# Performance work log

Hardware: AMD Instinct MI355X
Metric: run time of the kernel (lower is better)

Reference implementation:

```python
import jax, jax.numpy as jnp
import numpy as np

NUM_HEADS = 16

def setup_inputs() -> dict:
    key = jax.random.key(0)
    ks = jax.random.split(key, 7)
    B, Nq, Nkv, D = 4, 1024, 4096, 1024
    q = jax.random.normal(ks[0], (B, Nq, D), dtype=jnp.float32)
    kv = jax.random.normal(ks[1], (B, Nkv, D), dtype=jnp.float32)
    # True = padded key; keep position 0 unmasked so no row is fully masked
    mask = jax.random.randint(ks[2], (B, Nkv), 0, 2) > 0
    mask = mask.at[:, 0].set(False)
    s = D ** -0.5
    Wq = jax.random.normal(ks[3], (D, D), dtype=jnp.float32) * s
    Wkv = jax.random.normal(ks[4], (D, 2 * D), dtype=jnp.float32) * s
    Wproj = jax.random.normal(ks[5], (D, D), dtype=jnp.float32) * s
    bproj = jnp.zeros((D,), dtype=jnp.float32)
    return {"q": q, "kv": kv, "key_padding_mask": mask,
            "Wq": Wq, "Wkv": Wkv, "Wproj": Wproj, "bproj": bproj}

def reference(q, kv, key_padding_mask, Wq, Wkv, Wproj, bproj):
    B, Nq, D = q.shape
    Nkv = kv.shape[1]
    H = NUM_HEADS
    hd = D // H
    scale = hd ** -0.5
    # projections (qkv_bias=False)
    qp = (q @ Wq).reshape(B, Nq, H, hd).transpose(0, 2, 1, 3) * scale  # (B,H,Nq,hd)
    kvp = kv @ Wkv  # (B,Nkv,2D); first D -> k, last D -> v
    k = kvp[..., :D].reshape(B, Nkv, H, hd).transpose(0, 2, 1, 3)  # (B,H,Nkv,hd)
    v = kvp[..., D:].reshape(B, Nkv, H, hd).transpose(0, 2, 1, 3)
    attn = jnp.einsum('bhqd,bhkd->bhqk', qp, k)  # (B,H,Nq,Nkv)
    neg_inf = jnp.finfo(attn.dtype).min
    attn = jnp.where(key_padding_mask[:, None, None, :], neg_inf, attn)
    attn = jax.nn.softmax(attn, axis=-1)
    x = jnp.einsum('bhqk,bhkd->bhqd', attn, v)  # (B,H,Nq,hd)
    x = x.transpose(0, 2, 1, 3).reshape(B, Nq, D)
    return x @ Wproj + bproj
```

## Files before the change

kernel.cpp:

```cpp
#include <hip/hip_runtime.h>
#include <hip/hip_bf16.h>
#include <math.h>

#define BB 4
#define NQ 1024
#define NKV 4096
#define DMODEL 1024
#define NH 16
#define HD 64

typedef __attribute__((ext_vector_type(8))) short short8;
typedef __attribute__((ext_vector_type(4))) float floatx4;

__device__ __forceinline__ unsigned short f2bf(float f) {
    __hip_bfloat16 b = __float2bfloat16(f);
    return *reinterpret_cast<unsigned short*>(&b);
}

__device__ __forceinline__ unsigned int pack2bf_rhu(float a, float b) {
    unsigned ua = __builtin_bit_cast(unsigned, a) + 0x8000u;
    unsigned ub = __builtin_bit_cast(unsigned, b) + 0x8000u;
    return (ua >> 16) | (ub & 0xffff0000u);
}

__device__ __forceinline__ void gl_lds16(void* lds, const void* g) {
    __builtin_amdgcn_global_load_lds(
        (const __attribute__((address_space(1))) unsigned int*)g,
        (__attribute__((address_space(3))) unsigned int*)lds, 16, 0, 0);
}

__global__ __launch_bounds__(1024) void maskprep3(const int* __restrict__ mask,
                                                  unsigned short* __restrict__ maskb) {
    __shared__ int s;
    if (threadIdx.x == 0) s = 0;
    __syncthreads();
    int local = 0;
    for (int i = threadIdx.x; i < 4096; i += 1024)
        if (((const unsigned*)mask)[i] > 1u) local = 1;
    if (local) atomicOr(&s, 1);
    __syncthreads();
    const bool bytes = (s != 0);
    for (int i = threadIdx.x; i < BB * NKV; i += 1024) {
        bool m = bytes ? (((const unsigned char*)mask)[i] != 0) : (mask[i] != 0);
        maskb[i] = m ? (unsigned short)0 : (unsigned short)0xFFFFu;
    }
}

__global__ __launch_bounds__(256) void cast_bf16(const float* __restrict__ src,
                                                 unsigned short* __restrict__ dst,
                                                 int n) {
    int i = (blockIdx.x * 256 + threadIdx.x) * 8;
    if (i >= n) return;
    float4 a = *(const float4*)&src[i];
    float4 b = *(const float4*)&src[i + 4];
    short8 v;
    v[0] = (short)f2bf(a.x); v[1] = (short)f2bf(a.y);
    v[2] = (short)f2bf(a.z); v[3] = (short)f2bf(a.w);
    v[4] = (short)f2bf(b.x); v[5] = (short)f2bf(b.y);
    v[6] = (short)f2bf(b.z); v[7] = (short)f2bf(b.w);
    *(short8*)&dst[i] = v;
}

__global__ __launch_bounds__(256) void transpose_cast3(
    const float* __restrict__ Wq, const float* __restrict__ Wkv,
    const float* __restrict__ Wproj,
    unsigned short* __restrict__ WqT, unsigned short* __restrict__ WkvT,
    unsigned short* __restrict__ WprojT)
{
    const float* src; unsigned short* dst; int N;
    if (blockIdx.z == 0)      { src = Wq;    dst = WqT;    N = DMODEL; }
    else if (blockIdx.z == 1) { src = Wkv;   dst = WkvT;   N = 2 * DMODEL; }
    else                      { src = Wproj; dst = WprojT; N = DMODEL; }
    if ((int)blockIdx.x * 64 >= N) return;
    const int K = DMODEL;
    __shared__ unsigned short t[64][72];
    int r0 = blockIdx.y * 64, c0 = blockIdx.x * 64;
    int tid = threadIdx.x;
#pragma unroll
    for (int i = 0; i < 4; i++) {
        int r = i * 16 + (tid >> 4), c = (tid & 15) * 4;
        float4 v = *(const float4*)&src[(size_t)(r0 + r) * N + c0 + c];
        t[c + 0][r] = f2bf(v.x); t[c + 1][r] = f2bf(v.y);
        t[c + 2][r] = f2bf(v.z); t[c + 3][r] = f2bf(v.w);
    }
    __syncthreads();
#pragma unroll
    for (int i = 0; i < 2; i++) {
        int rr = i * 32 + (tid >> 3), cc = (tid & 7) * 8;
        *(uint4*)&dst[(size_t)(c0 + rr) * K + r0 + cc] = *(uint4*)&t[rr][cc];
    }
}

template <int EPI>
__global__ __launch_bounds__(256) void gemm_mfma(
    const unsigned short* __restrict__ A,
    const unsigned short* __restrict__ Bt,
    const float* __restrict__ bias,
    unsigned short* __restrict__ o16,
    unsigned short* __restrict__ oT,
    float* __restrict__ o32,
    int M, int N, int K, float alpha, int m_out_base)
{
    extern __shared__ char smem[];
    unsigned short* As = (unsigned short*)smem;
    unsigned short* Bs = (unsigned short*)(smem + 8192);
    const int tid = threadIdx.x;
    const int wave = tid >> 6, lane = tid & 63;
    const int quad = lane >> 4, l16 = lane & 15;
    const int wm = wave >> 1, wn = wave & 1;
    const int m0 = blockIdx.y * 128, n0 = blockIdx.x * 128;

    const int c0 = wave * 64 + lane, c1 = c0 + 256;
    const int r0s = c0 >> 2, cc0 = (c0 & 3) ^ ((r0s >> 2) & 3);
    const int r1s = c1 >> 2, cc1 = (c1 & 3) ^ ((r1s >> 2) & 3);
    const unsigned short* ag0 = A + (size_t)(m0 + r0s) * K + cc0 * 8;
    const unsigned short* ag1 = A + (size_t)(m0 + r1s) * K + cc1 * 8;
    const unsigned short* bg0 = Bt + (size_t)(n0 + r0s) * K + cc0 * 8;
    const unsigned short* bg1 = Bt + (size_t)(n0 + r1s) * K + cc1 * 8;
    char* AldsW0 = (char*)As + (wave * 64) * 16;
    char* AldsW1 = (char*)As + (256 + wave * 64) * 16;
    char* BldsW0 = (char*)Bs + (wave * 64) * 16;
    char* BldsW1 = (char*)Bs + (256 + wave * 64) * 16;

    int achk[4], bchk[4];
#pragma unroll
    for (int i = 0; i < 4; i++) {
        int ra = wm * 64 + i * 16 + l16;
        achk[i] = ra * 4 + (quad ^ ((ra >> 2) & 3));
        int rb = wn * 64 + i * 16 + l16;
        bchk[i] = rb * 4 + (quad ^ ((rb >> 2) & 3));
    }

    floatx4 acc[4][4];
#pragma unroll
    for (int i = 0; i < 4; i++)
#pragma unroll
        for (int j = 0; j < 4; j++) acc[i][j] = (floatx4)0.0f;

    for (int kt = 0; kt < K; kt += 32) {
        __syncthreads();
        gl_lds16(AldsW0, ag0 + kt);
        gl_lds16(AldsW1, ag1 + kt);
        gl_lds16(BldsW0, bg0 + kt);
        gl_lds16(BldsW1, bg1 + kt);
        __syncthreads();
        short8 af[4], bfr[4];
#pragma unroll
        for (int i = 0; i < 4; i++) af[i] = *(const short8*)&As[achk[i] * 8];
#pragma unroll
        for (int j = 0; j < 4; j++) bfr[j] = *(const short8*)&Bs[bchk[j] * 8];
#pragma unroll
        for (int i = 0; i < 4; i++)
#pragma unroll
            for (int j = 0; j < 4; j++)
                acc[i][j] = __builtin_amdgcn_mfma_f32_16x16x32_bf16(
                    af[i], bfr[j], acc[i][j], 0, 0, 0);
    }

    const int rowbase = m0 + wm * 64;
    const int colbase = n0 + wn * 64;
    if (EPI == 0) {
#pragma unroll
        for (int i = 0; i < 4; i++)
#pragma unroll
            for (int r = 0; r < 4; r++) {
                size_t row = (size_t)(rowbase + i * 16 + quad * 4 + r);
#pragma unroll
                for (int j = 0; j < 4; j++)
                    o16[row * N + colbase + j * 16 + l16] =
                        f2bf(acc[i][j][r] * alpha);
            }
    } else if (EPI == 2) {
        float bv[4];
#pragma unroll
        for (int j = 0; j < 4; j++) bv[j] = bias[colbase + j * 16 + l16];
#pragma unroll
        for (int i = 0; i < 4; i++)
#pragma unroll
            for (int r = 0; r < 4; r++) {
                size_t row = (size_t)(rowbase + i * 16 + quad * 4 + r);
#pragma unroll
                for (int j = 0; j < 4; j++)
                    o32[row * N + colbase + j * 16 + l16] = acc[i][j][r] + bv[j];
            }
    } else {
        if (n0 < DMODEL) {
#pragma unroll
            for (int i = 0; i < 4; i++)
#pragma unroll
                for (int r = 0; r < 4; r++) {
                    int gm = m_out_base + rowbase + i * 16 + quad * 4 + r;
                    int b = gm >> 12, key = gm & (NKV - 1);
                    size_t row = (size_t)(b * NKV + key);
#pragma unroll
                    for (int j = 0; j < 4; j++)
                        o16[row * DMODEL + colbase + j * 16 + l16] =
                            f2bf(acc[i][j][r]);
                }
        } else {
            __syncthreads();
            unsigned short (*scr)[72] =
                (unsigned short(*)[72])(smem + wave * 64 * 72 * 2);
#pragma unroll
            for (int i = 0; i < 4; i++)
#pragma unroll
                for (int j = 0; j < 4; j++)
#pragma unroll
                    for (int r = 0; r < 4; r++)
                        scr[j * 16 + l16][i * 16 + quad * 4 + r] =
                            f2bf(acc[i][j][r]);
            __syncthreads();
            int gmb = m_out_base + rowbase;
            int b = gmb >> 12, key0 = gmb & (NKV - 1);
            int d0 = colbase - DMODEL;
#pragma unroll
            for (int p = 0; p < 8; p++) {
                int rr = p * 8 + (lane >> 3), ch = lane & 7;
                *(uint4*)&oT[((size_t)(b * DMODEL + d0 + rr)) * NKV + key0 + ch * 8] =
                    *(uint4*)&scr[rr][ch * 8];
            }
        }
    }
}

__global__ __launch_bounds__(512, 2) void attn_mfma11(
    const unsigned short* __restrict__ Qb,
    const unsigned short* __restrict__ Kb,
    const unsigned short* __restrict__ VTb,
    const unsigned short* __restrict__ maskb,
    unsigned short* __restrict__ x)
{
    const int lid = blockIdx.y * gridDim.x + blockIdx.x;
    const int xcd = lid & 7, slot = lid >> 3;
    const int bh = xcd * 8 + (slot & 7);
    const int b = bh >> 4, h = bh & 15;
    const int m0 = (slot >> 3) * 128;
    const int tid = threadIdx.x;
    const int wave = tid >> 6, lane = tid & 63;
    const int quad = lane >> 4, l16 = lane & 15;
    const int sp = wave & 3;
    const int g  = wave >> 2;

    __shared__ __align__(16) char smem[55296];
    unsigned short (*k_s)[64][72]  = (unsigned short (*)[64][72])(smem);
    unsigned short (*vT_s)[64][72] = (unsigned short (*)[64][72])(smem + 18432);
    unsigned short (*qp_s)[16][72] = (unsigned short (*)[16][72])(smem + 36864);
    float* comb = (float*)smem;

    const unsigned short* Kbase = Kb + ((size_t)b * NKV) * DMODEL + h * HD;
    const unsigned short* Vbase = VTb + ((size_t)(b * DMODEL + h * HD)) * NKV;

    const int sg  = tid >> 8;
    const int t8  = tid & 255;
    const int sr  = t8 >> 2;
    const int sc  = (t8 & 3) * 16;
    const int key00 = sg * 2048;

    {
        const unsigned short* ks = Kbase + (size_t)(key00 + sr) * DMODEL + sc;
        uint4 a0 = *(const uint4*)ks, a1 = *(const uint4*)(ks + 8);
        const unsigned short* vs = Vbase + (size_t)sr * NKV + key00 + sc;
        uint4 b0 = *(const uint4*)vs, b1 = *(const uint4*)(vs + 8);
        *(uint4*)&k_s[sg][sr][sc]      = a0;
        *(uint4*)&k_s[sg][sr][sc + 8]  = a1;
        *(uint4*)&vT_s[sg][sr][sc]     = b0;
        *(uint4*)&vT_s[sg][sr][sc + 8] = b1;
    }

    short8 bq[2][2];
#pragma unroll
    for (int s = 0; s < 2; s++) {
        const unsigned short* qsrc =
            Qb + ((size_t)(b * NQ + m0 + sp * 32 + s * 16 + l16)) * DMODEL +
            h * HD + quad * 8;
        bq[s][0] = *(const short8*)qsrc;
        bq[s][1] = *(const short8*)(qsrc + 32);
    }

    const unsigned short* mrow = maskb + b * NKV + g * 2048;
    unsigned short* prow = &qp_s[wave][l16][0];

    short8 ones;
#pragma unroll
    for (int e = 0; e < 8; e++) ones[e] = (short)0x3F80;

    floatx4 o[2][4], ol[2];
#pragma unroll
    for (int s = 0; s < 2; s++) {
#pragma unroll
        for (int f = 0; f < 4; f++) o[s][f] = (floatx4)0.0f;
        ol[s] = (floatx4)0.0f;
    }

    __syncthreads();

    for (int i = 0; i < 32; i++) {
        if (i) __syncthreads();
        const bool pf = (i < 31);
        const int nn = key00 + (i + 1) * 64;

        uint4 pk0, pk1;
        if (pf) {
            const unsigned short* ks = Kbase + (size_t)(nn + sr) * DMODEL + sc;
            pk0 = *(const uint4*)ks; pk1 = *(const uint4*)(ks + 8);
        }

        floatx4 st[2][4];
        __builtin_amdgcn_s_setprio(1);
#pragma unroll
        for (int f = 0; f < 4; f++) {
            short8 ak0 = *(const short8*)&k_s[g][f * 16 + l16][quad * 8];
            short8 ak1 = *(const short8*)&k_s[g][f * 16 + l16][32 + quad * 8];
            floatx4 t0 = (floatx4)0.0f, t1 = (floatx4)0.0f;
            t0 = __builtin_amdgcn_mfma_f32_16x16x32_bf16(ak0, bq[0][0], t0, 0, 0, 0);
            t0 = __builtin_amdgcn_mfma_f32_16x16x32_bf16(ak1, bq[0][1], t0, 0, 0, 0);
            t1 = __builtin_amdgcn_mfma_f32_16x16x32_bf16(ak0, bq[1][0], t1, 0, 0, 0);
            t1 = __builtin_amdgcn_mfma_f32_16x16x32_bf16(ak1, bq[1][1], t1, 0, 0, 0);
            st[0][f] = t0; st[1][f] = t1;
        }
        __builtin_amdgcn_s_setprio(0);

        uint4 pv0, pv1;
        if (pf) {
            const unsigned short* vs = Vbase + (size_t)sr * NKV + nn + sc;
            pv0 = *(const uint4*)vs; pv1 = *(const uint4*)(vs + 8);
        }

        short8 ap[2][2];
#pragma unroll
        for (int s = 0; s < 2; s++) {
#pragma unroll
            for (int f = 0; f < 4; f++) {
                uint2 mwf = *(const uint2*)&mrow[i * 64 + f * 16 + quad * 4];
                float p0 = __builtin_amdgcn_exp2f(st[s][f][0]);
                float p1 = __builtin_amdgcn_exp2f(st[s][f][1]);
                float p2 = __builtin_amdgcn_exp2f(st[s][f][2]);
                float p3 = __builtin_amdgcn_exp2f(st[s][f][3]);
                uint2 pw;
                pw.x = pack2bf_rhu(p0, p1) & mwf.x;
                pw.y = pack2bf_rhu(p2, p3) & mwf.y;
                *(uint2*)&prow[f * 16 + quad * 4] = pw;
            }
            asm volatile("s_waitcnt lgkmcnt(0)" ::: "memory");
            ap[s][0] = *(const short8*)&prow[quad * 8];
            ap[s][1] = *(const short8*)&prow[32 + quad * 8];
        }

        __builtin_amdgcn_s_setprio(1);
#pragma unroll
        for (int f = 0; f < 4; f++) {
            short8 bv0 = *(const short8*)&vT_s[g][f * 16 + l16][quad * 8];
            short8 bv1 = *(const short8*)&vT_s[g][f * 16 + l16][32 + quad * 8];
            o[0][f] = __builtin_amdgcn_mfma_f32_16x16x32_bf16(ap[0][0], bv0, o[0][f], 0, 0, 0);
            o[0][f] = __builtin_amdgcn_mfma_f32_16x16x32_bf16(ap[0][1], bv1, o[0][f], 0, 0, 0);
            o[1][f] = __builtin_amdgcn_mfma_f32_16x16x32_bf16(ap[1][0], bv0, o[1][f], 0, 0, 0);
            o[1][f] = __builtin_amdgcn_mfma_f32_16x16x32_bf16(ap[1][1], bv1, o[1][f], 0, 0, 0);
        }
        ol[0] = __builtin_amdgcn_mfma_f32_16x16x32_bf16(ap[0][0], ones, ol[0], 0, 0, 0);
        ol[0] = __builtin_amdgcn_mfma_f32_16x16x32_bf16(ap[0][1], ones, ol[0], 0, 0, 0);
        ol[1] = __builtin_amdgcn_mfma_f32_16x16x32_bf16(ap[1][0], ones, ol[1], 0, 0, 0);
        ol[1] = __builtin_amdgcn_mfma_f32_16x16x32_bf16(ap[1][1], ones, ol[1], 0, 0, 0);
        __builtin_amdgcn_s_setprio(0);

        __syncthreads();
        if (pf) {
            *(uint4*)&k_s[sg][sr][sc]      = pk0;
            *(uint4*)&k_s[sg][sr][sc + 8]  = pk1;
            *(uint4*)&vT_s[sg][sr][sc]     = pv0;
            *(uint4*)&vT_s[sg][sr][sc + 8] = pv1;
        }
    }

    if (wave >= 4) {
        float* dst = comb + ((size_t)((wave - 4) * 64 + lane)) * 40;
#pragma unroll
        for (int s = 0; s < 2; s++)
#pragma unroll
            for (int f = 0; f < 4; f++)
                *(floatx4*)(dst + (s * 4 + f) * 4) = o[s][f];
        *(floatx4*)(dst + 32) = ol[0];
        *(floatx4*)(dst + 36) = ol[1];
    }
    __syncthreads();
    if (wave < 4) {
        const float* src = comb + ((size_t)(wave * 64 + lane)) * 40;
#pragma unroll
        for (int s = 0; s < 2; s++)
#pragma unroll
            for (int f = 0; f < 4; f++)
                o[s][f] += *(const floatx4*)(src + (s * 4 + f) * 4);
        ol[0] += *(const floatx4*)(src + 32);
        ol[1] += *(const floatx4*)(src + 36);

#pragma unroll
        for (int s = 0; s < 2; s++) {
#pragma unroll
            for (int r = 0; r < 4; r++) {
                float inv = 1.0f / ol[s][r];
                size_t row = (size_t)(b * NQ + m0 + wave * 32 + s * 16 + quad * 4 + r);
#pragma unroll
                for (int f = 0; f < 4; f++) {
                    unsigned u = __builtin_bit_cast(unsigned, o[s][f][r] * inv) + 0x8000u;
                    x[row * DMODEL + h * HD + f * 16 + l16] = (unsigned short)(u >> 16);
                }
            }
        }
    }
}

extern "C" void kernel_launch(void* const* d_in, const int* in_sizes, int n_in,
                              void* d_out, int out_size, void* d_ws, size_t ws_size,
                              hipStream_t stream) {
    const float* q     = (const float*)d_in[0];
    const float* kv    = (const float*)d_in[1];
    const int*   mask  = (const int*)d_in[2];
    const float* Wq    = (const float*)d_in[3];
    const float* Wkv   = (const float*)d_in[4];
    const float* Wproj = (const float*)d_in[5];
    const float* bproj = (const float*)d_in[6];
    float* out = (float*)d_out;

    char* ws = (char*)d_ws;
    size_t o = 0;
    o += 256;
    unsigned short* maskb  = (unsigned short*)(ws + o); o += 65536;
    unsigned short* Qb     = (unsigned short*)(ws + o); o += (size_t)BB * NQ * DMODEL * 2;
    unsigned short* Kb     = (unsigned short*)(ws + o); o += (size_t)BB * NKV * DMODEL * 2;
    unsigned short* VTb    = (unsigned short*)(ws + o); o += (size_t)BB * NKV * DMODEL * 2;
    unsigned short* WprojT = (unsigned short*)(ws + o); o += (size_t)DMODEL * DMODEL * 2;
    unsigned short* qbf    = (unsigned short*)(ws + o);
    unsigned short* xb     = qbf;
    o += (size_t)BB * NQ * DMODEL * 2;
    unsigned short* WqT    = (unsigned short*)(ws + o); o += (size_t)DMODEL * DMODEL * 2;
    unsigned short* WkvT   = (unsigned short*)(ws + o); o += (size_t)DMODEL * 2 * DMODEL * 2;
    unsigned short* kvh = (unsigned short*)d_out;

    hipLaunchKernelGGL(maskprep3, dim3(1), dim3(1024), 0, stream, mask, maskb);
    hipLaunchKernelGGL(transpose_cast3, dim3(32, DMODEL / 64, 3), dim3(256), 0, stream,
                       Wq, Wkv, Wproj, WqT, WkvT, WprojT);

    hipLaunchKernelGGL(cast_bf16, dim3(BB * NQ * DMODEL / 2048), dim3(256), 0, stream,
                       q, qbf, BB * NQ * DMODEL);
    hipLaunchKernelGGL((gemm_mfma<0>), dim3(DMODEL / 128, BB * NQ / 128), dim3(256), 16384, stream,
                       qbf, WqT, (const float*)nullptr, Qb, (unsigned short*)nullptr,
                       (float*)nullptr, BB * NQ, DMODEL, DMODEL, 0.125f * 1.44269504f, 0);

    const int HALF_ROWS = BB * NKV / 2;
    for (int half = 0; half < 2; half++) {
        const float* src = kv + (size_t)half * HALF_ROWS * DMODEL;
        hipLaunchKernelGGL(cast_bf16, dim3(HALF_ROWS * DMODEL / 2048), dim3(256), 0, stream,
                           src, kvh, HALF_ROWS * DMODEL);
        hipLaunchKernelGGL((gemm_mfma<1>), dim3(2 * DMODEL / 128, HALF_ROWS / 128), dim3(256), 36864, stream,
                           kvh, WkvT, (const float*)nullptr, Kb, VTb,
                           (float*)nullptr, HALF_ROWS, 2 * DMODEL, DMODEL, 1.0f, half * HALF_ROWS);
    }

    hipLaunchKernelGGL(attn_mfma11, dim3(NQ / 128, BB * NH), dim3(512), 0, stream,
                       Qb, Kb, VTb, maskb, xb);

    hipLaunchKernelGGL((gemm_mfma<2>), dim3(DMODEL / 128, BB * NQ / 128), dim3(256), 16384, stream,
                       xb, WprojT, bproj, (unsigned short*)nullptr, (unsigned short*)nullptr,
                       out, BB * NQ, DMODEL, DMODEL, 1.0f, 0);
}
```

Baseline: 405.0 us.

## Fuse fp32-to-bf16 input cast into projection GEMM loads and remap workgroups

The separate cast_bf16 passes over q and kv are removed. The Q and KV projection GEMMs now read fp32 activations directly, convert them to bf16 in registers and store them to LDS, which saves writing and re-reading a bf16 copy. The KV projection also becomes a single launch instead of two halves. A workgroup-ID remap spreads consecutive blocks across groups of eight, likely for cache or XCD locality. In exchange, the A-operand loads are now synchronous register loads rather than direct global-to-LDS copies, which may expose more load latency inside the K loop.

After: 415.9 us. +2.7%, slower.

```diff
diff --git a/kernel.cpp b/kernel.cpp
--- a/kernel.cpp
+++ b/kernel.cpp
@@ -44,21 +44,6 @@
         bool m = bytes ? (((const unsigned char*)mask)[i] != 0) : (mask[i] != 0);
         maskb[i] = m ? (unsigned short)0 : (unsigned short)0xFFFFu;
     }
-}
-
-__global__ __launch_bounds__(256) void cast_bf16(const float* __restrict__ src,
-                                                 unsigned short* __restrict__ dst,
-                                                 int n) {
-    int i = (blockIdx.x * 256 + threadIdx.x) * 8;
-    if (i >= n) return;
-    float4 a = *(const float4*)&src[i];
-    float4 b = *(const float4*)&src[i + 4];
-    short8 v;
-    v[0] = (short)f2bf(a.x); v[1] = (short)f2bf(a.y);
-    v[2] = (short)f2bf(a.z); v[3] = (short)f2bf(a.w);
-    v[4] = (short)f2bf(b.x); v[5] = (short)f2bf(b.y);
-    v[6] = (short)f2bf(b.z); v[7] = (short)f2bf(b.w);
-    *(short8*)&dst[i] = v;
 }
 
 __global__ __launch_bounds__(256) void transpose_cast3(
@@ -91,9 +76,10 @@
     }
 }
 
-template <int EPI>
+template <int EPI, int AF32>
 __global__ __launch_bounds__(256) void gemm_mfma(
     const unsigned short* __restrict__ A,
+    const float* __restrict__ A32,
     const unsigned short* __restrict__ Bt,
     const float* __restrict__ bias,
     unsigned short* __restrict__ o16,
@@ -108,19 +94,34 @@
     const int wave = tid >> 6, lane = tid & 63;
     const int quad = lane >> 4, l16 = lane & 15;
     const int wm = wave >> 1, wn = wave & 1;
-    const int m0 = blockIdx.y * 128, n0 = blockIdx.x * 128;
+
+    const int nwg = gridDim.x * gridDim.y;
+    const int lid0 = blockIdx.y * gridDim.x + blockIdx.x;
+    const int lid = (lid0 & 7) * (nwg >> 3) + (lid0 >> 3);
+    const int bx = lid % gridDim.x, by = lid / gridDim.x;
+    const int m0 = by * 128, n0 = bx * 128;
 
     const int c0 = wave * 64 + lane, c1 = c0 + 256;
     const int r0s = c0 >> 2, cc0 = (c0 & 3) ^ ((r0s >> 2) & 3);
     const int r1s = c1 >> 2, cc1 = (c1 & 3) ^ ((r1s >> 2) & 3);
-    const unsigned short* ag0 = A + (size_t)(m0 + r0s) * K + cc0 * 8;
-    const unsigned short* ag1 = A + (size_t)(m0 + r1s) * K + cc1 * 8;
     const unsigned short* bg0 = Bt + (size_t)(n0 + r0s) * K + cc0 * 8;
     const unsigned short* bg1 = Bt + (size_t)(n0 + r1s) * K + cc1 * 8;
     char* AldsW0 = (char*)As + (wave * 64) * 16;
     char* AldsW1 = (char*)As + (256 + wave * 64) * 16;
     char* BldsW0 = (char*)Bs + (wave * 64) * 16;
     char* BldsW1 = (char*)Bs + (256 + wave * 64) * 16;
+    char* Alane0 = (char*)As + c0 * 16;
+    char* Alane1 = (char*)As + c1 * 16;
+
+    const unsigned short* ag0 = nullptr; const unsigned short* ag1 = nullptr;
+    const float* ag0f = nullptr; const float* ag1f = nullptr;
+    if constexpr (AF32) {
+        ag0f = A32 + (size_t)(m0 + r0s) * K + cc0 * 8;
+        ag1f = A32 + (size_t)(m0 + r1s) * K + cc1 * 8;
+    } else {
+        ag0 = A + (size_t)(m0 + r0s) * K + cc0 * 8;
+        ag1 = A + (size_t)(m0 + r1s) * K + cc1 * 8;
+    }
 
     int achk[4], bchk[4];
 #pragma unroll
@@ -139,10 +140,30 @@
 
     for (int kt = 0; kt < K; kt += 32) {
         __syncthreads();
-        gl_lds16(AldsW0, ag0 + kt);
-        gl_lds16(AldsW1, ag1 + kt);
-        gl_lds16(BldsW0, bg0 + kt);
-        gl_lds16(BldsW1, bg1 + kt);
+        if constexpr (AF32) {
+            float4 x0 = *(const float4*)(ag0f + kt);
+            float4 x1 = *(const float4*)(ag0f + kt + 4);
+            float4 x2 = *(const float4*)(ag1f + kt);
+            float4 x3 = *(const float4*)(ag1f + kt + 4);
+            gl_lds16(BldsW0, bg0 + kt);
+            gl_lds16(BldsW1, bg1 + kt);
+            short8 v0, v1;
+            v0[0] = (short)f2bf(x0.x); v0[1] = (short)f2bf(x0.y);
+            v0[2] = (short)f2bf(x0.z); v0[3] = (short)f2bf(x0.w);
+            v0[4] = (short)f2bf(x1.x); v0[5] = (short)f2bf(x1.y);
+            v0[6] = (short)f2bf(x1.z); v0[7] = (short)f2bf(x1.w);
+            v1[0] = (short)f2bf(x2.x); v1[1] = (short)f2bf(x2.y);
+            v1[2] = (short)f2bf(x2.z); v1[3] = (short)f2bf(x2.w);
+            v1[4] = (short)f2bf(x3.x); v1[5] = (short)f2bf(x3.y);
+            v1[6] = (short)f2bf(x3.z); v1[7] = (short)f2bf(x3.w);
+            *(short8*)Alane0 = v0;
+            *(short8*)Alane1 = v1;
+        } else {
+            gl_lds16(AldsW0, ag0 + kt);
+            gl_lds16(AldsW1, ag1 + kt);
+            gl_lds16(BldsW0, bg0 + kt);
+            gl_lds16(BldsW1, bg1 + kt);
+        }
         __syncthreads();
         short8 af[4], bfr[4];
 #pragma unroll
@@ -428,37 +449,30 @@
     unsigned short* Kb     = (unsigned short*)(ws + o); o += (size_t)BB * NKV * DMODEL * 2;
     unsigned short* VTb    = (unsigned short*)(ws + o); o += (size_t)BB * NKV * DMODEL * 2;
     unsigned short* WprojT = (unsigned short*)(ws + o); o += (size_t)DMODEL * DMODEL * 2;
-    unsigned short* qbf    = (unsigned short*)(ws + o);
-    unsigned short* xb     = qbf;
+    unsigned short* xb     = (unsigned short*)(ws + o);
     o += (size_t)BB * NQ * DMODEL * 2;
     unsigned short* WqT    = (unsigned short*)(ws + o); o += (size_t)DMODEL * DMODEL * 2;
     unsigned short* WkvT   = (unsigned short*)(ws + o); o += (size_t)DMODEL * 2 * DMODEL * 2;
-    unsigned short* kvh = (unsigned short*)d_out;
 
     hipLaunchKernelGGL(maskprep3, dim3(1), dim3(1024), 0, stream, mask, maskb);
     hipLaunchKernelGGL(transpose_cast3, dim3(32, DMODEL / 64, 3), dim3(256), 0, stream,
                        Wq, Wkv, Wproj, WqT, WkvT, WprojT);
 
-    hipLaunchKernelGGL(cast_bf16, dim3(BB * NQ * DMODEL / 2048), dim3(256), 0, stream,
-                       q, qbf, BB * NQ * DMODEL);
-    hipLaunchKernelGGL((gemm_mfma<0>), dim3(DMODEL / 128, BB * NQ / 128), dim3(256), 16384, stream,
-                       qbf, WqT, (const float*)nullptr, Qb, (unsigned short*)nullptr,
-                       (float*)nullptr, BB * NQ, DMODEL, DMODEL, 0.125f * 1.44269504f, 0);
-
-    const int HALF_ROWS = BB * NKV / 2;
-    for (int half = 0; half < 2; half++) {
-        const float* src = kv + (size_t)half * HALF_ROWS * DMODEL;
-        hipLaunchKernelGGL(cast_bf16, dim3(HALF_ROWS * DMODEL / 2048), dim3(256), 0, stream,
-                           src, kvh, HALF_ROWS * DMODEL);
-        hipLaunchKernelGGL((gemm_mfma<1>), dim3(2 * DMODEL / 128, HALF_ROWS / 128), dim3(256), 36864, stream,
-                           kvh, WkvT, (const float*)nullptr, Kb, VTb,
-                           (float*)nullptr, HALF_ROWS, 2 * DMODEL, DMODEL, 1.0f, half * HALF_ROWS);
-    }
+    hipLaunchKernelGGL((gemm_mfma<0, 1>), dim3(DMODEL / 128, BB * NQ / 128), dim3(256), 16384, stream,
+                       (const unsigned short*)nullptr, q, WqT, (const float*)nullptr,
+                       Qb, (unsigned short*)nullptr, (float*)nullptr,
+                       BB * NQ, DMODEL, DMODEL, 0.125f * 1.44269504f, 0);
+
+    hipLaunchKernelGGL((gemm_mfma<1, 1>), dim3(2 * DMODEL / 128, BB * NKV / 128), dim3(256), 36864, stream,
+                       (const unsigned short*)nullptr, kv, WkvT, (const float*)nullptr,
+                       Kb, VTb, (float*)nullptr,
+                       BB * NKV, 2 * DMODEL, DMODEL, 1.0f, 0);
 
     hipLaunchKernelGGL(attn_mfma11, dim3(NQ / 128, BB * NH), dim3(512), 0, stream,
                        Qb, Kb, VTb, maskb, xb);
 
-    hipLaunchKernelGGL((gemm_mfma<2>), dim3(DMODEL / 128, BB * NQ / 128), dim3(256), 16384, stream,
-                       xb, WprojT, bproj, (unsigned short*)nullptr, (unsigned short*)nullptr,
-                       out, BB * NQ, DMODEL, DMODEL, 1.0f, 0);
-}
+    hipLaunchKernelGGL((gemm_mfma<2, 0>), dim3(DMODEL / 128, BB * NQ / 128), dim3(256), 16384, stream,
+                       xb, (const float*)nullptr, WprojT, bproj,
+                       (unsigned short*)nullptr, (unsigned short*)nullptr, out,
+                       BB * NQ, DMODEL, DMODEL, 1.0f, 0);
+}
```
